# Kernel tuning notes

Measured on AMD Instinct MI355X. Metric: run time of the kernel, lower is better.

The kernel has to match this reference:

```python
import jax, jax.numpy as jnp
import numpy as np

C = 384
HEADS = 8
HEAD_DIM = C // HEADS
BN_EPS = 1e-5


def _bn(x, g, b, m, v):
    # inference-mode BatchNorm2d over channel dim (NCHW)
    inv = jax.lax.rsqrt(v + BN_EPS)
    return (x - m[None, :, None, None]) * (inv * g)[None, :, None, None] + b[None, :, None, None]


def _conv1x1(x, w, b):
    # w: [out, in]; x: [B, in, H, W]
    return jnp.einsum('oc,bchw->bohw', w, x) + b[None, :, None, None]


def setup_inputs() -> dict:
    key = jax.random.key(0)
    ks = jax.random.split(key, 12)
    s = 0.02
    inp = {
        'x': jax.random.normal(ks[0], (16, C, 28, 28), dtype=jnp.float32),
        'local_w': jax.random.normal(ks[1], (C, 1, 3, 3), dtype=jnp.float32) * (1.0 / 3.0),
        'local_b': jnp.zeros((C,), jnp.float32),
        'bn1_g': jnp.ones((C,), jnp.float32),
        'bn1_b': jnp.zeros((C,), jnp.float32),
        'bn1_m': jnp.zeros((C,), jnp.float32),
        'bn1_v': jnp.ones((C,), jnp.float32),
        'q_w': jax.random.normal(ks[2], (C, C), dtype=jnp.float32) * s,
        'q_b': jnp.zeros((C,), jnp.float32),
        'k_w': jax.random.normal(ks[3], (C, C), dtype=jnp.float32) * s,
        'k_b': jnp.zeros((C,), jnp.float32),
        'v_w': jax.random.normal(ks[4], (C, C), dtype=jnp.float32) * s,
        'v_b': jnp.zeros((C,), jnp.float32),
        'proj_w': jax.random.normal(ks[5], (C, C), dtype=jnp.float32) * s,
        'proj_b': jnp.zeros((C,), jnp.float32),
        'ffn1_w': jax.random.normal(ks[6], (4 * C, C), dtype=jnp.float32) * s,
        'ffn1_b': jnp.zeros((4 * C,), jnp.float32),
        'ffn2_w': jax.random.normal(ks[7], (C, 4 * C), dtype=jnp.float32) * s,
        'ffn2_b': jnp.zeros((C,), jnp.float32),
        'bn2_g': jnp.ones((C,), jnp.float32),
        'bn2_b': jnp.zeros((C,), jnp.float32),
        'bn2_m': jnp.zeros((C,), jnp.float32),
        'bn2_v': jnp.ones((C,), jnp.float32),
    }
    return inp


def reference(x, local_w, local_b, bn1_g, bn1_b, bn1_m, bn1_v,
              q_w, q_b, k_w, k_b, v_w, v_b, proj_w, proj_b,
              ffn1_w, ffn1_b, ffn2_w, ffn2_b, bn2_g, bn2_b, bn2_m, bn2_v):
    B, Cc, H, W = x.shape
    N = H * W
    # depthwise 3x3 conv + BN (eval mode)
    lx = jax.lax.conv_general_dilated(
        x, local_w, window_strides=(1, 1), padding='SAME',
        feature_group_count=Cc,
        dimension_numbers=('NCHW', 'OIHW', 'NCHW')) + local_b[None, :, None, None]
    lx = _bn(lx, bn1_g, bn1_b, bn1_m, bn1_v)

    # QKV via 1x1 convs, split into heads over flattened tokens
    q = _conv1x1(lx, q_w, q_b).reshape(B, HEADS, HEAD_DIM, N).transpose(0, 1, 3, 2)  # bhnd
    k = _conv1x1(lx, k_w, k_b).reshape(B, HEADS, HEAD_DIM, N)                          # bhdm
    v = _conv1x1(lx, v_w, v_b).reshape(B, HEADS, HEAD_DIM, N).transpose(0, 1, 3, 2)  # bhmd

    attn = jax.nn.softmax(jnp.einsum('bhnd,bhdm->bhnm', q, k) * (HEAD_DIM ** -0.5), axis=-1)
    out = jnp.einsum('bhnm,bhmd->bhnd', attn, v)
    out = out.transpose(0, 1, 3, 2).reshape(B, Cc, H, W)

    out = _conv1x1(out, proj_w, proj_b) + lx
    residual = out
    h = _bn(out, bn2_g, bn2_b, bn2_m, bn2_v)
    h = _conv1x1(h, ffn1_w, ffn1_b)
    h = jax.nn.gelu(h, approximate=False)
    h = _conv1x1(h, ffn2_w, ffn2_b)
    return h + residual
```

## Files before the change

### kernel.cpp

```cpp
#include <hip/hip_runtime.h>
#include <hip/hip_bf16.h>
#include <math.h>

#define BATCH 16
#define CH 384
#define HH 28
#define WW 28
#define NTOK 784
#define NTOT (BATCH * NTOK)
#define NHEADS 8
#define HDIM 48
#define C4 1536
#define QKVC 1152
#define BN_EPS 1e-5f
#define QTL 128
#define KTL 64
#define WCC (CH * CH)
#define NW_ALL (4 * WCC + 2 * C4 * CH)
#define LAMBDA (0.14433756729740643f * 1.4426950408889634f)
#define VT_BSTRIDE 832
#define VT_CSTRIDE (16 * 832)

typedef __attribute__((ext_vector_type(8))) short bf16x8;
typedef __attribute__((ext_vector_type(4))) float f32x4;

__device__ __forceinline__ void async16(void* lds, const void* g) {
  __builtin_amdgcn_global_load_lds(
      (const __attribute__((address_space(1))) void*)g,
      (__attribute__((address_space(3))) void*)lds, 16, 0, 0);
}
__device__ __forceinline__ float bf2f(__hip_bfloat16 v) { return __bfloat162float(v); }
__device__ __forceinline__ ushort f2bf_bits(float f) {
  __hip_bfloat16 t = __float2bfloat16(f);
  return *reinterpret_cast<ushort*>(&t);
}

__global__ __launch_bounds__(256) void zero_vt_tail(__hip_bfloat16* __restrict__ vt) {
  const bf16x8 z8 = {0, 0, 0, 0, 0, 0, 0, 0};
  int i = blockIdx.x * 256 + threadIdx.x;
  if (i < CH * BATCH * 8) {
    int chunk = i & 7, cb = i >> 3;
    int ch = cb >> 4, b = cb & 15;
    *(bf16x8*)(vt + (size_t)ch * VT_CSTRIDE + b * VT_BSTRIDE + 768 + chunk * 8) = z8;
  }
}

__global__ __launch_bounds__(256) void cvt_all(
    const float* __restrict__ q_w, const float* __restrict__ k_w,
    const float* __restrict__ v_w, const float* __restrict__ proj_w,
    const float* __restrict__ ffn1_w, const float* __restrict__ ffn2_w,
    const float* __restrict__ g, const float* __restrict__ vv,
    const float* __restrict__ qb, const float* __restrict__ kb,
    const float* __restrict__ vb,
    __hip_bfloat16* __restrict__ wdst, float* __restrict__ qkvb) {
  int i = blockIdx.x * 256 + threadIdx.x;
  if (i < QKVC) {
    float bvv;
    if (i < CH) bvv = qb[i] * LAMBDA;
    else if (i < 2 * CH) bvv = kb[i - CH];
    else bvv = vb[i - 2 * CH];
    qkvb[i] = bvv;
  }
  if (i < NW_ALL) {
    float val;
    if (i < WCC) val = q_w[i] * LAMBDA;
    else if (i < 2 * WCC) val = k_w[i - WCC];
    else if (i < 3 * WCC) val = v_w[i - 2 * WCC];
    else if (i < 4 * WCC) val = proj_w[i - 3 * WCC];
    else if (i < 4 * WCC + C4 * CH) {
      int j = i - 4 * WCC;
      int c = j % CH;
      val = ffn1_w[j] * g[c] * rsqrtf(vv[c] + BN_EPS);
    } else {
      val = ffn2_w[i - 4 * WCC - C4 * CH];
    }
    wdst[i] = __float2bfloat16(val);
  }
}

__global__ __launch_bounds__(256) void prep_bias2(
    const float* __restrict__ ffn1_w, const float* __restrict__ ffn1_b,
    const float* __restrict__ g, const float* __restrict__ bb,
    const float* __restrict__ m, const float* __restrict__ v,
    float* __restrict__ fbias) {
  int w = threadIdx.x >> 6, lane = threadIdx.x & 63;
  int o = blockIdx.x * 4 + w;
  float acc = 0.f;
  for (int c = lane; c < CH; c += 64) {
    float s = g[c] * rsqrtf(v[c] + BN_EPS);
    acc += ffn1_w[(size_t)o * CH + c] * (bb[c] - m[c] * s);
  }
#pragma unroll
  for (int off = 32; off; off >>= 1) acc += __shfl_xor(acc, off, 64);
  if (lane == 0) fbias[o] = ffn1_b[o] + acc;
}

__global__ __launch_bounds__(256) void dwconv_bn(
    const float* __restrict__ x, const float* __restrict__ w,
    const float* __restrict__ cb, const float* __restrict__ g,
    const float* __restrict__ bnb, const float* __restrict__ m,
    const float* __restrict__ var, float* __restrict__ lx) {
  int bc = blockIdx.x;
  int c = bc % CH;
  const float* xp = x + (size_t)bc * NTOK;
  float* op = lx + (size_t)bc * NTOK;
  float k[9];
#pragma unroll
  for (int i = 0; i < 9; ++i) k[i] = w[c * 9 + i];
  float s = g[c] * rsqrtf(var[c] + BN_EPS);
  float sh = (cb[c] - m[c]) * s + bnb[c];
  for (int n = threadIdx.x; n < NTOK; n += 256) {
    int y = n / WW, xx = n - y * WW;
    float acc = 0.f;
#pragma unroll
    for (int ky = -1; ky <= 1; ++ky) {
      int yy = y + ky;
      if (yy < 0 || yy >= HH) continue;
#pragma unroll
      for (int kx = -1; kx <= 1; ++kx) {
        int x2 = xx + kx;
        if (x2 < 0 || x2 >= WW) continue;
        acc += k[(ky + 1) * 3 + (kx + 1)] * xp[yy * WW + x2];
      }
    }
    op[n] = acc * s + sh;
  }
}

__global__ __launch_bounds__(256) void transpose_cvt(
    const float* __restrict__ in, __hip_bfloat16* __restrict__ outb) {
  __shared__ float t[32][33];
  int b = blockIdx.z, c0 = blockIdx.y * 32, n0 = blockIdx.x * 32;
  int tx = threadIdx.x & 31, ty = threadIdx.x >> 5;
  for (int cc = ty; cc < 32; cc += 8) {
    int n = n0 + tx;
    t[cc][tx] = (n < NTOK) ? in[((size_t)b * CH + c0 + cc) * NTOK + n] : 0.f;
  }
  __syncthreads();
  for (int nn = ty; nn < 32; nn += 8) {
    int n = n0 + nn;
    if (n < NTOK) outb[((size_t)b * NTOK + n) * CH + c0 + tx] = __float2bfloat16(t[tx][nn]);
  }
}

template <int EPI>
__global__ __launch_bounds__(256) void gemm_mfma(
    const __hip_bfloat16* __restrict__ Arows, const __hip_bfloat16* __restrict__ Brows,
    const float* __restrict__ bias, const __hip_bfloat16* __restrict__ resid,
    void* __restrict__ outp, void* __restrict__ outp2, int K) {
  __shared__ __align__(16) ushort As[128 * 32];
  __shared__ __align__(16) ushort Bs[128 * 32];
  const int tid = threadIdx.x;
  const int w = tid >> 6;
  const int lane = tid & 63;
  const int quad = lane >> 4;
  const int l16 = lane & 15;
  const int m0 = blockIdx.y * 128;
  const int n0 = blockIdx.x * 128;
  const int wm = (w & 1) * 64, wn = (w >> 1) * 64;
  const int NB = gridDim.x * 128;
  const int MB = gridDim.y * 128;

  f32x4 zero = {0.f, 0.f, 0.f, 0.f};
  f32x4 acc[4][4];
#pragma unroll
  for (int i = 0; i < 4; ++i)
#pragma unroll
    for (int j = 0; j < 4; ++j) acc[i][j] = zero;

  for (int k0 = 0; k0 < K; k0 += 32) {
    __syncthreads();
#pragma unroll
    for (int t = 0; t < 2; ++t) {
      int c = w * 128 + t * 64 + lane;
      int row = c >> 2;
      int sg = (c & 3) ^ ((c >> 3) & 3);
      async16(As + (size_t)(w * 128 + t * 64) * 8,
              Arows + (size_t)(m0 + row) * K + k0 + sg * 8);
    }
#pragma unroll
    for (int t = 0; t < 2; ++t) {
      int c = w * 128 + t * 64 + lane;
      int row = c >> 2;
      int sg = (c & 3) ^ ((c >> 3) & 3);
      async16(Bs + (size_t)(w * 128 + t * 64) * 8,
              Brows + (size_t)(n0 + row) * K + k0 + sg * 8);
    }
    __syncthreads();

    bf16x8 af[4], bf[4];
#pragma unroll
    for (int i = 0; i < 4; ++i) {
      int ra = wm + i * 16 + l16;
      int sa = quad ^ ((ra >> 1) & 3);
      af[i] = *(const bf16x8*)&As[ra * 32 + sa * 8];
      int rb = wn + i * 16 + l16;
      int sb = quad ^ ((rb >> 1) & 3);
      bf[i] = *(const bf16x8*)&Bs[rb * 32 + sb * 8];
    }
#pragma unroll
    for (int i = 0; i < 4; ++i)
#pragma unroll
      for (int j = 0; j < 4; ++j)
        acc[i][j] = __builtin_amdgcn_mfma_f32_16x16x32_bf16(af[i], bf[j], acc[i][j], 0, 0, 0);
  }

#pragma unroll
  for (int i = 0; i < 4; ++i) {
#pragma unroll
    for (int j = 0; j < 4; ++j) {
#pragma unroll
      for (int r = 0; r < 4; ++r) {
        int mrow = m0 + wm + i * 16 + quad * 4 + r;
        int ncol = n0 + wn + j * 16 + l16;
        float val = acc[i][j][r];
        if (EPI == 0) {
          val += bias[ncol];
          if (ncol < 2 * CH) {
            ((__hip_bfloat16*)outp)[(size_t)mrow * (2 * CH) + ncol] = __float2bfloat16(val);
          } else {
            int ch = ncol - 2 * CH;
            int bq = mrow / NTOK;
            int tb = mrow - bq * NTOK;
            int tt = tb & 63, t64 = tb >> 6;
            int phi = ((tt & 15) << 2) | (tt >> 4);
            ((__hip_bfloat16*)outp2)[(size_t)ch * VT_CSTRIDE + bq * VT_BSTRIDE + t64 * 64 + phi] =
                __float2bfloat16(val);
          }
        } else if (EPI <= 2) {
          val += bias[ncol];
          if (EPI == 1) val += bf2f(resid[(size_t)mrow * NB + ncol]);
          if (EPI == 2) val = 0.5f * val * (1.f + erff(val * 0.70710678118654752f));
          ((__hip_bfloat16*)outp)[(size_t)mrow * NB + ncol] = __float2bfloat16(val);
        } else {
          val += bias[mrow];
          val += bf2f(resid[(size_t)ncol * MB + mrow]);
          int bq = ncol / NTOK, nn = ncol - bq * NTOK;
          ((float*)outp)[((size_t)bq * MB + mrow) * NTOK + nn] = val;
        }
      }
    }
  }
}

__global__ __launch_bounds__(256) void attention_mfma2(
    const __hip_bfloat16* __restrict__ qk, const __hip_bfloat16* __restrict__ vt,
    __hip_bfloat16* __restrict__ ob) {
  __shared__ __align__(16) ushort Ks[KTL][72];
  __shared__ __align__(16) ushort Vts[HDIM][72];
  __shared__ __align__(16) ushort Ps[4][32][72];

  const int tid = threadIdx.x;
  const int w = tid >> 6, lane = tid & 63;
  const int quad = lane >> 4, l16 = lane & 15;
  const int h = blockIdx.y, b = blockIdx.z;
  const int n0 = blockIdx.x * QTL;
  const size_t tokbase = (size_t)b * NTOK;
  const bf16x8 z8 = {0, 0, 0, 0, 0, 0, 0, 0};

  bf16x8 aq[2][2];
#pragma unroll
  for (int s = 0; s < 2; ++s) {
    int tok = n0 + w * 32 + s * 16 + l16;
    if (tok >= NTOK) tok = NTOK - 1;
#pragma unroll
    for (int kk = 0; kk < 2; ++kk)
      aq[s][kk] = *(const bf16x8*)(qk + (tokbase + tok) * (2 * CH) + h * HDIM + kk * 32 + quad * 8);
    if (quad >= 2) aq[s][1] = z8;
  }

  bf16x8 kreg[2], vreg[2];
  auto loadK = [&](int m0k) {
#pragma unroll
    for (int t = 0; t < 2; ++t) {
      int c = tid + t * 256;
      int row = c >> 3, hc = c & 7;
      int tok = m0k + row;
      bf16x8 val = z8;
      if (hc < 6 && tok < NTOK)
        val = *(const bf16x8*)(qk + (tokbase + tok) * (2 * CH) + CH + h * HDIM + hc * 8);
      kreg[t] = val;
    }
  };
  auto loadV = [&](int m0k) {
#pragma unroll
    for (int t = 0; t < 2; ++t) {
      int c = tid + t * 256;
      if (c < HDIM * 8) {
        int d = c >> 3, hc = c & 7;
        vreg[t] = *(const bf16x8*)(vt + (size_t)(h * HDIM + d) * VT_CSTRIDE + b * VT_BSTRIDE + m0k + hc * 8);
      }
    }
  };

  float m_i[2][4], l_i[2][4];
#pragma unroll
  for (int s = 0; s < 2; ++s)
#pragma unroll
    for (int r = 0; r < 4; ++r) { m_i[s][r] = -1e30f; l_i[s][r] = 0.f; }
  f32x4 o[2][3];
  const f32x4 zf = {0.f, 0.f, 0.f, 0.f};
#pragma unroll
  for (int s = 0; s < 2; ++s)
#pragma unroll
    for (int t = 0; t < 3; ++t) o[s][t] = zf;

  loadK(0);
  loadV(0);

  for (int m0 = 0; m0 < NTOK; m0 += KTL) {
    __syncthreads();
#pragma unroll
    for (int t = 0; t < 2; ++t) {
      int c = tid + t * 256;
      *(bf16x8*)&Ks[c >> 3][(c & 7) * 8] = kreg[t];
    }
#pragma unroll
    for (int t = 0; t < 2; ++t) {
      int c = tid + t * 256;
      if (c < HDIM * 8) *(bf16x8*)&Vts[c >> 3][(c & 7) * 8] = vreg[t];
    }
    __syncthreads();
    int mn = m0 + KTL;
    if (mn < NTOK) { loadK(mn); loadV(mn); }

    f32x4 sa[2][4];
#pragma unroll
    for (int s = 0; s < 2; ++s)
#pragma unroll
      for (int j = 0; j < 4; ++j) sa[s][j] = zf;
#pragma unroll
    for (int kk = 0; kk < 2; ++kk) {
#pragma unroll
      for (int j = 0; j < 4; ++j) {
        bf16x8 kf = *(const bf16x8*)&Ks[j * 16 + l16][kk * 32 + quad * 8];
        sa[0][j] = __builtin_amdgcn_mfma_f32_16x16x32_bf16(aq[0][kk], kf, sa[0][j], 0, 0, 0);
        sa[1][j] = __builtin_amdgcn_mfma_f32_16x16x32_bf16(aq[1][kk], kf, sa[1][j], 0, 0, 0);
      }
    }

    const bool lastT = (m0 + KTL > NTOK);
    float alpha[2][4];
#pragma unroll
    for (int s = 0; s < 2; ++s) {
#pragma unroll
      for (int r = 0; r < 4; ++r) {
        float sv0 = sa[s][0][r], sv1 = sa[s][1][r], sv2 = sa[s][2][r], sv3 = sa[s][3][r];
        if (lastT) {
          if (m0 + 0 * 16 + l16 >= NTOK) sv0 = -1e30f;
          if (m0 + 1 * 16 + l16 >= NTOK) sv1 = -1e30f;
          if (m0 + 2 * 16 + l16 >= NTOK) sv2 = -1e30f;
          if (m0 + 3 * 16 + l16 >= NTOK) sv3 = -1e30f;
        }
        float mx = fmaxf(fmaxf(sv0, sv1), fmaxf(sv2, sv3));
#pragma unroll
        for (int off = 1; off < 16; off <<= 1) mx = fmaxf(mx, __shfl_xor(mx, off, 16));
        float mnew = fmaxf(m_i[s][r], mx);
        float al = __builtin_amdgcn_exp2f(m_i[s][r] - mnew);
        alpha[s][r] = al;
        m_i[s][r] = mnew;
        float p0 = __builtin_amdgcn_exp2f(sv0 - mnew);
        float p1 = __builtin_amdgcn_exp2f(sv1 - mnew);
        float p2 = __builtin_amdgcn_exp2f(sv2 - mnew);
        float p3 = __builtin_amdgcn_exp2f(sv3 - mnew);
        float sum = (p0 + p1) + (p2 + p3);
        int prow = s * 16 + quad * 4 + r;
        Ps[w][prow][4 * l16 + 0] = f2bf_bits(p0);
        Ps[w][prow][4 * l16 + 1] = f2bf_bits(p1);
        Ps[w][prow][4 * l16 + 2] = f2bf_bits(p2);
        Ps[w][prow][4 * l16 + 3] = f2bf_bits(p3);
#pragma unroll
        for (int off = 1; off < 16; off <<= 1) sum += __shfl_xor(sum, off, 16);
        l_i[s][r] = l_i[s][r] * al + sum;
      }
    }
#pragma unroll
    for (int s = 0; s < 2; ++s)
#pragma unroll
      for (int t = 0; t < 3; ++t)
#pragma unroll
        for (int r = 0; r < 4; ++r) o[s][t][r] *= alpha[s][r];

    __syncthreads();

    bf16x8 pf[2][2];
#pragma unroll
    for (int s = 0; s < 2; ++s)
#pragma unroll
      for (int kk = 0; kk < 2; ++kk)
        pf[s][kk] = *(const bf16x8*)&Ps[w][s * 16 + l16][kk * 32 + quad * 8];
#pragma unroll
    for (int kk = 0; kk < 2; ++kk) {
#pragma unroll
      for (int t = 0; t < 3; ++t) {
        bf16x8 vf = *(const bf16x8*)&Vts[t * 16 + l16][kk * 32 + quad * 8];
        o[0][t] = __builtin_amdgcn_mfma_f32_16x16x32_bf16(pf[0][kk], vf, o[0][t], 0, 0, 0);
        o[1][t] = __builtin_amdgcn_mfma_f32_16x16x32_bf16(pf[1][kk], vf, o[1][t], 0, 0, 0);
      }
    }
  }

#pragma unroll
  for (int s = 0; s < 2; ++s) {
    float inv[4];
#pragma unroll
    for (int r = 0; r < 4; ++r) inv[r] = __builtin_amdgcn_rcpf(l_i[s][r]);
#pragma unroll
    for (int t = 0; t < 3; ++t) {
#pragma unroll
      for (int r = 0; r < 4; ++r) {
        int tok = n0 + w * 32 + s * 16 + quad * 4 + r;
        if (tok < NTOK)
          ob[(tokbase + tok) * CH + h * HDIM + t * 16 + l16] =
              __float2bfloat16(o[s][t][r] * inv[r]);
      }
    }
  }
}

extern "C" void kernel_launch(void* const* d_in, const int* in_sizes, int n_in,
                              void* d_out, int out_size, void* d_ws, size_t ws_size,
                              hipStream_t stream) {
  const float* x       = (const float*)d_in[0];
  const float* local_w = (const float*)d_in[1];
  const float* local_b = (const float*)d_in[2];
  const float* bn1_g   = (const float*)d_in[3];
  const float* bn1_b   = (const float*)d_in[4];
  const float* bn1_m   = (const float*)d_in[5];
  const float* bn1_v   = (const float*)d_in[6];
  const float* q_w     = (const float*)d_in[7];
  const float* q_b     = (const float*)d_in[8];
  const float* k_w     = (const float*)d_in[9];
  const float* k_b     = (const float*)d_in[10];
  const float* v_w     = (const float*)d_in[11];
  const float* v_b     = (const float*)d_in[12];
  const float* proj_w  = (const float*)d_in[13];
  const float* proj_b  = (const float*)d_in[14];
  const float* ffn1_w  = (const float*)d_in[15];
  const float* ffn1_b  = (const float*)d_in[16];
  const float* ffn2_w  = (const float*)d_in[17];
  const float* ffn2_b  = (const float*)d_in[18];
  const float* bn2_g   = (const float*)d_in[19];
  const float* bn2_b   = (const float*)d_in[20];
  const float* bn2_m   = (const float*)d_in[21];
  const float* bn2_v   = (const float*)d_in[22];

  char* wsb = (char*)d_ws;
  float*          lx_cm   = (float*)(wsb + 0);
  __hip_bfloat16* vt      = (__hip_bfloat16*)(wsb + 0);
  __hip_bfloat16* qk_act  = (__hip_bfloat16*)(wsb + 19267584);
  __hip_bfloat16* gelu_a  = (__hip_bfloat16*)(wsb + 0);
  __hip_bfloat16* attn_a  = (__hip_bfloat16*)(wsb + 48168960);
  __hip_bfloat16* lx_tm   = (__hip_bfloat16*)(wsb + 57802752);
  __hip_bfloat16* resid_a = (__hip_bfloat16*)(wsb + 67436544);
  __hip_bfloat16* w_qkv   = (__hip_bfloat16*)(wsb + 77070336);
  __hip_bfloat16* w_proj  = (__hip_bfloat16*)(wsb + 77955072);
  __hip_bfloat16* w_ffn1  = (__hip_bfloat16*)(wsb + 78249984);
  __hip_bfloat16* w_ffn2  = (__hip_bfloat16*)(wsb + 79429632);
  float*          b_qkv   = (float*)(wsb + 80609280);
  float*          b_ffn1  = (float*)(wsb + 80613888);

  cvt_all<<<dim3((NW_ALL + 255) / 256), dim3(256), 0, stream>>>(
      q_w, k_w, v_w, proj_w, ffn1_w, ffn2_w, bn2_g, bn2_v, q_b, k_b, v_b,
      w_qkv, b_qkv);
  prep_bias2<<<dim3(C4 / 4), dim3(256), 0, stream>>>(
      ffn1_w, ffn1_b, bn2_g, bn2_b, bn2_m, bn2_v, b_ffn1);

  dwconv_bn<<<dim3(BATCH * CH), dim3(256), 0, stream>>>(
      x, local_w, local_b, bn1_g, bn1_b, bn1_m, bn1_v, lx_cm);
  transpose_cvt<<<dim3(25, 12, BATCH), dim3(256), 0, stream>>>(lx_cm, lx_tm);

  zero_vt_tail<<<dim3((CH * BATCH * 8 + 255) / 256), dim3(256), 0, stream>>>(vt);

  gemm_mfma<0><<<dim3(QKVC / 128, NTOT / 128), dim3(256), 0, stream>>>(
      lx_tm, w_qkv, b_qkv, nullptr, qk_act, vt, CH);

  attention_mfma2<<<dim3((NTOK + QTL - 1) / QTL, NHEADS, BATCH), dim3(256), 0, stream>>>(
      qk_act, vt, attn_a);

  gemm_mfma<1><<<dim3(CH / 128, NTOT / 128), dim3(256), 0, stream>>>(
      attn_a, w_proj, proj_b, lx_tm, resid_a, nullptr, CH);

  gemm_mfma<2><<<dim3(C4 / 128, NTOT / 128), dim3(256), 0, stream>>>(
      resid_a, w_ffn1, b_ffn1, nullptr, gelu_a, nullptr, CH);

  gemm_mfma<3><<<dim3(NTOT / 128, CH / 128), dim3(256), 0, stream>>>(
      w_ffn2, gelu_a, ffn2_b, resid_a, d_out, nullptr, C4);
}
```

Baseline: 377.9 us.

## Merge prep kernels, store dwconv output as bf16, shrink tiles for narrow GEMMs

Folds the vt-tail zeroing and the ffn1 bias reduction into the weight-conversion kernel, so there are fewer launches. The depthwise conv now writes bf16 directly, which halves the bytes the transpose reads and drops its conversion. The GEMM is templated on tile sizes, and the proj and ffn2 GEMMs use 128x64 or 64x128 tiles to launch more blocks on the narrow 384-wide outputs. vt is moved to its own workspace region so it no longer aliases the conv output.

```diff
diff --git a/kernel.cpp b/kernel.cpp
--- a/kernel.cpp
+++ b/kernel.cpp
@@ -35,24 +35,16 @@
   return *reinterpret_cast<ushort*>(&t);
 }
 
-__global__ __launch_bounds__(256) void zero_vt_tail(__hip_bfloat16* __restrict__ vt) {
-  const bf16x8 z8 = {0, 0, 0, 0, 0, 0, 0, 0};
-  int i = blockIdx.x * 256 + threadIdx.x;
-  if (i < CH * BATCH * 8) {
-    int chunk = i & 7, cb = i >> 3;
-    int ch = cb >> 4, b = cb & 15;
-    *(bf16x8*)(vt + (size_t)ch * VT_CSTRIDE + b * VT_BSTRIDE + 768 + chunk * 8) = z8;
-  }
-}
-
 __global__ __launch_bounds__(256) void cvt_all(
     const float* __restrict__ q_w, const float* __restrict__ k_w,
     const float* __restrict__ v_w, const float* __restrict__ proj_w,
     const float* __restrict__ ffn1_w, const float* __restrict__ ffn2_w,
     const float* __restrict__ g, const float* __restrict__ vv,
     const float* __restrict__ qb, const float* __restrict__ kb,
-    const float* __restrict__ vb,
-    __hip_bfloat16* __restrict__ wdst, float* __restrict__ qkvb) {
+    const float* __restrict__ vb, const float* __restrict__ fb1,
+    const float* __restrict__ bb2, const float* __restrict__ mm2,
+    __hip_bfloat16* __restrict__ wdst, float* __restrict__ qkvb,
+    float* __restrict__ fbias, __hip_bfloat16* __restrict__ vtp) {
   int i = blockIdx.x * 256 + threadIdx.x;
   if (i < QKVC) {
     float bvv;
@@ -60,6 +52,12 @@
     else if (i < 2 * CH) bvv = kb[i - CH];
     else bvv = vb[i - 2 * CH];
     qkvb[i] = bvv;
+  }
+  if (i < CH * BATCH * 8) {
+    const bf16x8 z8 = {0, 0, 0, 0, 0, 0, 0, 0};
+    int chunk = i & 7, cb = i >> 3;
+    int ch = cb >> 4, b = cb & 15;
+    *(bf16x8*)(vtp + (size_t)ch * VT_CSTRIDE + b * VT_BSTRIDE + 768 + chunk * 8) = z8;
   }
   if (i < NW_ALL) {
     float val;
@@ -76,34 +74,29 @@
     }
     wdst[i] = __float2bfloat16(val);
   }
-}
-
-__global__ __launch_bounds__(256) void prep_bias2(
-    const float* __restrict__ ffn1_w, const float* __restrict__ ffn1_b,
-    const float* __restrict__ g, const float* __restrict__ bb,
-    const float* __restrict__ m, const float* __restrict__ v,
-    float* __restrict__ fbias) {
-  int w = threadIdx.x >> 6, lane = threadIdx.x & 63;
-  int o = blockIdx.x * 4 + w;
-  float acc = 0.f;
-  for (int c = lane; c < CH; c += 64) {
-    float s = g[c] * rsqrtf(v[c] + BN_EPS);
-    acc += ffn1_w[(size_t)o * CH + c] * (bb[c] - m[c] * s);
-  }
-#pragma unroll
-  for (int off = 32; off; off >>= 1) acc += __shfl_xor(acc, off, 64);
-  if (lane == 0) fbias[o] = ffn1_b[o] + acc;
+  if (blockIdx.x < C4 / 4) {
+    int w = threadIdx.x >> 6, lane = threadIdx.x & 63;
+    int o = blockIdx.x * 4 + w;
+    float acc = 0.f;
+    for (int c = lane; c < CH; c += 64) {
+      float s = g[c] * rsqrtf(vv[c] + BN_EPS);
+      acc += ffn1_w[(size_t)o * CH + c] * (bb2[c] - mm2[c] * s);
+    }
+#pragma unroll
+    for (int off = 32; off; off >>= 1) acc += __shfl_xor(acc, off, 64);
+    if (lane == 0) fbias[o] = fb1[o] + acc;
+  }
 }
 
 __global__ __launch_bounds__(256) void dwconv_bn(
     const float* __restrict__ x, const float* __restrict__ w,
     const float* __restrict__ cb, const float* __restrict__ g,
     const float* __restrict__ bnb, const float* __restrict__ m,
-    const float* __restrict__ var, float* __restrict__ lx) {
+    const float* __restrict__ var, __hip_bfloat16* __restrict__ lx) {
   int bc = blockIdx.x;
   int c = bc % CH;
   const float* xp = x + (size_t)bc * NTOK;
-  float* op = lx + (size_t)bc * NTOK;
+  __hip_bfloat16* op = lx + (size_t)bc * NTOK;
   float k[9];
 #pragma unroll
   for (int i = 0; i < 9; ++i) k[i] = w[c * 9 + i];
@@ -123,92 +116,98 @@
         acc += k[(ky + 1) * 3 + (kx + 1)] * xp[yy * WW + x2];
       }
     }
-    op[n] = acc * s + sh;
-  }
-}
-
-__global__ __launch_bounds__(256) void transpose_cvt(
-    const float* __restrict__ in, __hip_bfloat16* __restrict__ outb) {
-  __shared__ float t[32][33];
+    op[n] = __float2bfloat16(acc * s + sh);
+  }
+}
+
+__global__ __launch_bounds__(256) void transpose_b(
+    const ushort* __restrict__ in, ushort* __restrict__ outb) {
+  __shared__ ushort t[32][34];
   int b = blockIdx.z, c0 = blockIdx.y * 32, n0 = blockIdx.x * 32;
   int tx = threadIdx.x & 31, ty = threadIdx.x >> 5;
   for (int cc = ty; cc < 32; cc += 8) {
     int n = n0 + tx;
-    t[cc][tx] = (n < NTOK) ? in[((size_t)b * CH + c0 + cc) * NTOK + n] : 0.f;
+    t[cc][tx] = (n < NTOK) ? in[((size_t)b * CH + c0 + cc) * NTOK + n] : (ushort)0;
   }
   __syncthreads();
   for (int nn = ty; nn < 32; nn += 8) {
     int n = n0 + nn;
-    if (n < NTOK) outb[((size_t)b * NTOK + n) * CH + c0 + tx] = __float2bfloat16(t[tx][nn]);
-  }
-}
-
-template <int EPI>
+    if (n < NTOK) outb[((size_t)b * NTOK + n) * CH + c0 + tx] = t[tx][nn];
+  }
+}
+
+template <int EPI, int TM, int TN>
 __global__ __launch_bounds__(256) void gemm_mfma(
     const __hip_bfloat16* __restrict__ Arows, const __hip_bfloat16* __restrict__ Brows,
     const float* __restrict__ bias, const __hip_bfloat16* __restrict__ resid,
     void* __restrict__ outp, void* __restrict__ outp2, int K) {
-  __shared__ __align__(16) ushort As[128 * 32];
-  __shared__ __align__(16) ushort Bs[128 * 32];
+  constexpr int NI = TM / 32, NJ = TN / 32;
+  __shared__ __align__(16) ushort As[TM * 32];
+  __shared__ __align__(16) ushort Bs[TN * 32];
   const int tid = threadIdx.x;
   const int w = tid >> 6;
   const int lane = tid & 63;
   const int quad = lane >> 4;
   const int l16 = lane & 15;
-  const int m0 = blockIdx.y * 128;
-  const int n0 = blockIdx.x * 128;
-  const int wm = (w & 1) * 64, wn = (w >> 1) * 64;
-  const int NB = gridDim.x * 128;
-  const int MB = gridDim.y * 128;
+  const int m0 = blockIdx.y * TM;
+  const int n0 = blockIdx.x * TN;
+  const int wm = (w & 1) * (TM / 2), wn = (w >> 1) * (TN / 2);
+  const int NB = gridDim.x * TN;
+  const int MB = gridDim.y * TM;
 
   f32x4 zero = {0.f, 0.f, 0.f, 0.f};
-  f32x4 acc[4][4];
-#pragma unroll
-  for (int i = 0; i < 4; ++i)
-#pragma unroll
-    for (int j = 0; j < 4; ++j) acc[i][j] = zero;
+  f32x4 acc[NI][NJ];
+#pragma unroll
+  for (int i = 0; i < NI; ++i)
+#pragma unroll
+    for (int j = 0; j < NJ; ++j) acc[i][j] = zero;
 
   for (int k0 = 0; k0 < K; k0 += 32) {
     __syncthreads();
 #pragma unroll
-    for (int t = 0; t < 2; ++t) {
-      int c = w * 128 + t * 64 + lane;
+    for (int it = 0; it < (TM * 4 + 255) / 256; ++it) {
+      int cbase = it * 256 + w * 64;
+      int c = cbase + lane;
       int row = c >> 2;
       int sg = (c & 3) ^ ((c >> 3) & 3);
-      async16(As + (size_t)(w * 128 + t * 64) * 8,
+      async16(As + (size_t)cbase * 8,
               Arows + (size_t)(m0 + row) * K + k0 + sg * 8);
     }
 #pragma unroll
-    for (int t = 0; t < 2; ++t) {
-      int c = w * 128 + t * 64 + lane;
+    for (int it = 0; it < (TN * 4 + 255) / 256; ++it) {
+      int cbase = it * 256 + w * 64;
+      int c = cbase + lane;
       int row = c >> 2;
       int sg = (c & 3) ^ ((c >> 3) & 3);
-      async16(Bs + (size_t)(w * 128 + t * 64) * 8,
+      async16(Bs + (size_t)cbase * 8,
               Brows + (size_t)(n0 + row) * K + k0 + sg * 8);
     }
     __syncthreads();
 
-    bf16x8 af[4], bf[4];
-#pragma unroll
-    for (int i = 0; i < 4; ++i) {
+    bf16x8 af[NI], bf[NJ];
+#pragma unroll
+    for (int i = 0; i < NI; ++i) {
       int ra = wm + i * 16 + l16;
       int sa = quad ^ ((ra >> 1) & 3);
       af[i] = *(const bf16x8*)&As[ra * 32 + sa * 8];
-      int rb = wn + i * 16 + l16;
+    }
+#pragma unroll
+    for (int j = 0; j < NJ; ++j) {
+      int rb = wn + j * 16 + l16;
       int sb = quad ^ ((rb >> 1) & 3);
-      bf[i] = *(const bf16x8*)&Bs[rb * 32 + sb * 8];
-    }
-#pragma unroll
-    for (int i = 0; i < 4; ++i)
-#pragma unroll
-      for (int j = 0; j < 4; ++j)
+      bf[j] = *(const bf16x8*)&Bs[rb * 32 + sb * 8];
+    }
+#pragma unroll
+    for (int i = 0; i < NI; ++i)
+#pragma unroll
+      for (int j = 0; j < NJ; ++j)
         acc[i][j] = __builtin_amdgcn_mfma_f32_16x16x32_bf16(af[i], bf[j], acc[i][j], 0, 0, 0);
   }
 
 #pragma unroll
-  for (int i = 0; i < 4; ++i) {
-#pragma unroll
-    for (int j = 0; j < 4; ++j) {
+  for (int i = 0; i < NI; ++i) {
+#pragma unroll
+    for (int j = 0; j < NJ; ++j) {
 #pragma unroll
       for (int r = 0; r < 4; ++r) {
         int mrow = m0 + wm + i * 16 + quad * 4 + r;
@@ -446,10 +445,9 @@
   const float* bn2_v   = (const float*)d_in[22];
 
   char* wsb = (char*)d_ws;
-  float*          lx_cm   = (float*)(wsb + 0);
-  __hip_bfloat16* vt      = (__hip_bfloat16*)(wsb + 0);
+  __hip_bfloat16* lx_cmb  = (__hip_bfloat16*)(wsb + 0);
+  __hip_bfloat16* gelu_a  = (__hip_bfloat16*)(wsb + 0);
   __hip_bfloat16* qk_act  = (__hip_bfloat16*)(wsb + 19267584);
-  __hip_bfloat16* gelu_a  = (__hip_bfloat16*)(wsb + 0);
   __hip_bfloat16* attn_a  = (__hip_bfloat16*)(wsb + 48168960);
   __hip_bfloat16* lx_tm   = (__hip_bfloat16*)(wsb + 57802752);
   __hip_bfloat16* resid_a = (__hip_bfloat16*)(wsb + 67436544);
@@ -459,31 +457,29 @@
   __hip_bfloat16* w_ffn2  = (__hip_bfloat16*)(wsb + 79429632);
   float*          b_qkv   = (float*)(wsb + 80609280);
   float*          b_ffn1  = (float*)(wsb + 80613888);
+  __hip_bfloat16* vt      = (__hip_bfloat16*)(wsb + 85000192);
 
   cvt_all<<<dim3((NW_ALL + 255) / 256), dim3(256), 0, stream>>>(
       q_w, k_w, v_w, proj_w, ffn1_w, ffn2_w, bn2_g, bn2_v, q_b, k_b, v_b,
-      w_qkv, b_qkv);
-  prep_bias2<<<dim3(C4 / 4), dim3(256), 0, stream>>>(
-      ffn1_w, ffn1_b, bn2_g, bn2_b, bn2_m, bn2_v, b_ffn1);
+      ffn1_b, bn2_b, bn2_m, w_qkv, b_qkv, b_ffn1, vt);
 
   dwconv_bn<<<dim3(BATCH * CH), dim3(256), 0, stream>>>(
-      x, local_w, local_b, bn1_g, bn1_b, bn1_m, bn1_v, lx_cm);
-  transpose_cvt<<<dim3(25, 12, BATCH), dim3(256), 0, stream>>>(lx_cm, lx_tm);
-
-  zero_vt_tail<<<dim3((CH * BATCH * 8 + 255) / 256), dim3(256), 0, stream>>>(vt);
-
-  gemm_mfma<0><<<dim3(QKVC / 128, NTOT / 128), dim3(256), 0, stream>>>(
+      x, local_w, local_b, bn1_g, bn1_b, bn1_m, bn1_v, lx_cmb);
+  transpose_b<<<dim3(25, 12, BATCH), dim3(256), 0, stream>>>(
+      (const ushort*)lx_cmb, (ushort*)lx_tm);
+
+  gemm_mfma<0, 128, 128><<<dim3(QKVC / 128, NTOT / 128), dim3(256), 0, stream>>>(
       lx_tm, w_qkv, b_qkv, nullptr, qk_act, vt, CH);
 
   attention_mfma2<<<dim3((NTOK + QTL - 1) / QTL, NHEADS, BATCH), dim3(256), 0, stream>>>(
       qk_act, vt, attn_a);
 
-  gemm_mfma<1><<<dim3(CH / 128, NTOT / 128), dim3(256), 0, stream>>>(
+  gemm_mfma<1, 128, 64><<<dim3(CH / 64, NTOT / 128), dim3(256), 0, stream>>>(
       attn_a, w_proj, proj_b, lx_tm, resid_a, nullptr, CH);
 
-  gemm_mfma<2><<<dim3(C4 / 128, NTOT / 128), dim3(256), 0, stream>>>(
+  gemm_mfma<2, 128, 128><<<dim3(C4 / 128, NTOT / 128), dim3(256), 0, stream>>>(
       resid_a, w_ffn1, b_ffn1, nullptr, gelu_a, nullptr, CH);
 
-  gemm_mfma<3><<<dim3(NTOT / 128, CH / 128), dim3(256), 0, stream>>>(
+  gemm_mfma<3, 64, 128><<<dim3(NTOT / 128, CH / 64), dim3(256), 0, stream>>>(
       w_ffn2, gelu_a, ffn2_b, resid_a, d_out, nullptr, C4);
 }
```

After: 365.8 us. -3.2%, faster.
